# Kernel optimization log

Hardware: AMD Instinct MI355X
Metric: run time of the kernel (lower is better)

The kernel has to match this reference:

```python
import jax, jax.numpy as jnp
import numpy as np

N_NODES = 100000
N_EDGES = 1600000
F_IN, F_HID, F_OUT = 64, 64, 32


def setup_inputs() -> dict:
    key = jax.random.key(0)
    k1, k2, k3, k4 = jax.random.split(key, 4)
    x = jax.random.normal(k1, (N_NODES, F_IN), dtype=jnp.float32)
    edge_idx = jax.random.randint(k2, (2, N_EDGES), 0, N_NODES, dtype=jnp.int64)
    W1 = jax.random.normal(k3, (F_IN, F_HID), dtype=jnp.float32) * (1.0 / np.sqrt(F_IN))
    b1 = jnp.zeros((F_HID,), dtype=jnp.float32)
    W2 = jax.random.normal(k4, (F_HID, F_OUT), dtype=jnp.float32) * (1.0 / np.sqrt(F_HID))
    b2 = jnp.zeros((F_OUT,), dtype=jnp.float32)
    return {"x": x, "edge_idx": edge_idx, "W1": W1, "b1": b1, "W2": W2, "b2": b2}


def _gcn_conv(h, src, dst, norm, W, b, n):
    # PyG GCNConv: transform first, then normalized sum aggregation, then bias.
    h = h @ W                                   # [N, F_out]
    msg = h[src] * norm[:, None]                # [E+N, F_out] gather + scale
    agg = jax.ops.segment_sum(msg, dst, num_segments=n)  # scatter-add
    return agg + b


def reference(x, edge_idx, W1, b1, W2, b2):
    n = x.shape[0]
    loop = jnp.arange(n, dtype=edge_idx.dtype)
    src = jnp.concatenate([edge_idx[0], loop])  # add self-loops
    dst = jnp.concatenate([edge_idx[1], loop])
    # symmetric normalization D^-1/2 (A+I) D^-1/2
    deg = jax.ops.segment_sum(jnp.ones_like(dst, dtype=x.dtype), dst, num_segments=n)
    dinv = jnp.where(deg > 0, jax.lax.rsqrt(deg), 0.0)
    norm = dinv[src] * dinv[dst]                # [E+N]

    h = _gcn_conv(x, src, dst, norm, W1, b1, n)
    h = jax.nn.relu(h)
    # dropout(p=0.5) is identity in eval mode (deterministic reference)
    out = _gcn_conv(h, src, dst, norm, W2, b2, n)
    return out
```

## Files before the change

### kernel.cpp

```cpp
#include <hip/hip_runtime.h>
#include <hip/hip_bf16.h>
#include <hip/hip_fp16.h>


#define N_FEAT_IN 64
#define B2SHIFT 9
#define CHUNK 4096
#define PADSTRIDE 3592

struct alignas(8) half4 { __half2 lo, hi; };
struct alignas(16) half8 { __half2 h[4]; };

__global__ __launch_bounds__(1024) void passA_hist(const int* __restrict__ dst,
                                                   int* __restrict__ H, int E) {
    __shared__ int h[256];
    int t = threadIdx.x;
    if (t < 256) h[t] = 0;
    __syncthreads();
    int base = blockIdx.x * CHUNK;
    int end = min(base + CHUNK, E);
    for (int i = base + t; i < end; i += 1024)
        atomicAdd(&h[dst[i] >> B2SHIFT], 1);
    __syncthreads();
    if (t < 256) H[blockIdx.x * 256 + t] = h[t];
}

__global__ __launch_bounds__(512) void col_scan_a(int* __restrict__ H,
                                                  int* __restrict__ ctot, int NR) {
    __shared__ int s[512];
    int b = blockIdx.x;
    int t = threadIdx.x;
    int v = (t < NR) ? H[t * 256 + b] : 0;
    s[t] = v;
    __syncthreads();
    for (int off = 1; off < 512; off <<= 1) {
        int a = (t >= off) ? s[t - off] : 0;
        __syncthreads();
        s[t] += a;
        __syncthreads();
    }
    if (t < NR) H[t * 256 + b] = s[t] - v;
    if (t == 511) ctot[b] = s[511];
}

__global__ __launch_bounds__(256) void col_scan_b(const int* __restrict__ ctot,
                                                  int* __restrict__ cbase,
                                                  int* __restrict__ bbase,
                                                  int* __restrict__ row_ptr,
                                                  int NB, int n, int E) {
    __shared__ int s[256];
    int t = threadIdx.x;
    int v = ctot[t];
    s[t] = v;
    __syncthreads();
    for (int off = 1; off < 256; off <<= 1) {
        int a = (t >= off) ? s[t - off] : 0;
        __syncthreads();
        s[t] += a;
        __syncthreads();
    }
    int e = s[t] - v;
    cbase[t] = e;
    if (t < NB) bbase[t] = e;
    if (t == 0) { bbase[NB] = E; row_ptr[n] = E; }
}

__global__ __launch_bounds__(1024) void passB_place(const int* __restrict__ src,
                                                    const int* __restrict__ dst,
                                                    const int* __restrict__ H,
                                                    const int* __restrict__ cbase,
                                                    unsigned* __restrict__ bedges, int E) {
    __shared__ int cur[256];
    int t = threadIdx.x;
    if (t < 256) cur[t] = H[blockIdx.x * 256 + t] + cbase[t];
    __syncthreads();
    int base = blockIdx.x * CHUNK;
    int end = min(base + CHUNK, E);
    for (int i = base + t; i < end; i += 1024) {
        int d = dst[i];
        int p = atomicAdd(&cur[d >> B2SHIFT], 1);
        bedges[p] = ((unsigned)src[i] << B2SHIFT) | (unsigned)(d & 511);
    }
}

__global__ __launch_bounds__(1024) void bucket_csr(const int* __restrict__ bbase,
                                                   const unsigned* __restrict__ bedges,
                                                   int* __restrict__ row_ptr,
                                                   int* __restrict__ rend,
                                                   float* __restrict__ dinv,
                                                   int* __restrict__ csr_src, int n) {
    __shared__ int lh[512];
    __shared__ int cur[512];
    int t = threadIdx.x;
    if (t < 512) lh[t] = 0;
    __syncthreads();
    int b = blockIdx.x;
    int beg = bbase[b], end = bbase[b + 1];
    for (int i = beg + t; i < end; i += 1024)
        atomicAdd(&lh[bedges[i] & 511], 1);
    __syncthreads();
    int c = (t < 512) ? lh[t] : 0;
    __syncthreads();
    int cp = (c + 7) & ~7;
    if (t < 512) lh[t] = cp;
    __syncthreads();
    for (int off = 1; off < 512; off <<= 1) {
        int a = (t < 512 && t >= off) ? lh[t - off] : 0;
        __syncthreads();
        if (t < 512) lh[t] += a;
        __syncthreads();
    }
    int pb = ((beg + 7) & ~7) + b * PADSTRIDE;
    if (t < 512) {
        int d = (b << B2SHIFT) + t;
        int rbeg = pb + lh[t] - cp;
        cur[t] = rbeg;
        if (d < n) {
            row_ptr[d] = rbeg;
            rend[d] = rbeg + cp;
            dinv[d] = rsqrtf((float)c + 1.0f);
            for (int i = c; i < cp; ++i) csr_src[rbeg + i] = n;
        }
    }
    __syncthreads();
    for (int i = beg + t; i < end; i += 1024) {
        unsigned v = bedges[i];
        int p = atomicAdd(&cur[v & 511], 1);
        csr_src[p] = (int)(v >> B2SHIFT);
    }
}

__global__ __launch_bounds__(256) void gemm64(const float* __restrict__ A,
                                              const float* __restrict__ W,
                                              const float* __restrict__ dinv,
                                              __half* __restrict__ outh, int n) {
    constexpr int K = 64, FO = 64, CPT = 16;
    __shared__ float As[64][K + 4];
    __shared__ float Ws[K][FO];

    const int t = threadIdx.x;
    const int r0 = blockIdx.x * 64;

    if (blockIdx.x == 0 && t < FO)
        outh[(size_t)n * FO + t] = __float2half(0.f);

    for (int i = t; i < K * FO / 4; i += 256) {
        int k = i / (FO / 4);
        int c4 = (i % (FO / 4)) * 4;
        *(float4*)&Ws[k][c4] = *(const float4*)&W[k * FO + c4];
    }
    for (int i = t; i < 1024; i += 256) {
        int row = i / 16;
        int c4 = (i % 16) * 4;
        int g = r0 + row;
        float4 v = make_float4(0.f, 0.f, 0.f, 0.f);
        if (g < n) v = *(const float4*)&A[(size_t)g * K + c4];
        *(float4*)&As[row][c4] = v;
    }
    __syncthreads();

    const int row = t >> 2;
    const int c0 = (t & 3) * CPT;
    float acc[CPT];
#pragma unroll
    for (int j = 0; j < CPT; ++j) acc[j] = 0.f;
#pragma unroll
    for (int k = 0; k < K; ++k) {
        float xv = As[row][k];
#pragma unroll
        for (int j = 0; j < CPT; ++j) acc[j] = fmaf(xv, Ws[k][c0 + j], acc[j]);
    }

    int g = r0 + row;
    if (g < n) {
        float sc = dinv[g];
#pragma unroll
        for (int j4 = 0; j4 < CPT; j4 += 4) {
            half4 h;
            h.lo = __floats2half2_rn(acc[j4] * sc, acc[j4 + 1] * sc);
            h.hi = __floats2half2_rn(acc[j4 + 2] * sc, acc[j4 + 3] * sc);
            *(half4*)&outh[(size_t)g * FO + c0 + j4] = h;
        }
    }
}

#define ACC8(v)                                                       \
    {                                                                 \
        float2 f0 = __half22float2((v).h[0]);                         \
        float2 f1 = __half22float2((v).h[1]);                         \
        float2 f2 = __half22float2((v).h[2]);                         \
        float2 f3 = __half22float2((v).h[3]);                         \
        a0 += f0.x; a1 += f0.y; a2 += f1.x; a3 += f1.y;               \
        a4 += f2.x; a5 += f2.y; a6 += f3.x; a7 += f3.y;               \
    }

__global__ __launch_bounds__(256) void agg64(const int* __restrict__ row_ptr,
                                             const int* __restrict__ rend,
                                             const int* __restrict__ csr_src,
                                             const float* __restrict__ dinv,
                                             const __half* __restrict__ xs1,
                                             const float* __restrict__ b1,
                                             __half* __restrict__ th, int n) {
    int d = blockIdx.x * 32 + (threadIdx.x >> 3);
    if (d >= n) return;
    int c = threadIdx.x & 7;
    const half8* __restrict__ xrow = (const half8*)xs1 + c;

    half8 sv = xrow[(size_t)d * 8];
    float a0, a1, a2, a3, a4, a5, a6, a7;
    {
        float2 f0 = __half22float2(sv.h[0]), f1 = __half22float2(sv.h[1]);
        float2 f2 = __half22float2(sv.h[2]), f3 = __half22float2(sv.h[3]);
        a0 = f0.x; a1 = f0.y; a2 = f1.x; a3 = f1.y;
        a4 = f2.x; a5 = f2.y; a6 = f3.x; a7 = f3.y;
    }

    int beg = row_ptr[d];
    int end = rend[d];
    if (beg < end) {
        int4 ia = *(const int4*)&csr_src[beg];
        int4 ib = *(const int4*)&csr_src[beg + 4];
        int jb = beg;
        for (;;) {
            int jn = jb + 8;
            bool more = jn < end;
            int js = more ? jn : beg;
            int4 na = *(const int4*)&csr_src[js];
            int4 nb = *(const int4*)&csr_src[js + 4];
            half8 v0 = xrow[(size_t)ia.x * 8];
            half8 v1 = xrow[(size_t)ia.y * 8];
            half8 v2 = xrow[(size_t)ia.z * 8];
            half8 v3 = xrow[(size_t)ia.w * 8];
            half8 v4 = xrow[(size_t)ib.x * 8];
            half8 v5 = xrow[(size_t)ib.y * 8];
            half8 v6 = xrow[(size_t)ib.z * 8];
            half8 v7 = xrow[(size_t)ib.w * 8];
            ACC8(v0); ACC8(v1); ACC8(v2); ACC8(v3);
            ACC8(v4); ACC8(v5); ACC8(v6); ACC8(v7);
            if (!more) break;
            jb = jn; ia = na; ib = nb;
        }
    }

    float di = dinv[d];
    float4 ba = *(const float4*)&b1[8 * c];
    float4 bb = *(const float4*)&b1[8 * c + 4];
    float t0 = fmaxf(fmaf(di, a0, ba.x), 0.f);
    float t1 = fmaxf(fmaf(di, a1, ba.y), 0.f);
    float t2 = fmaxf(fmaf(di, a2, ba.z), 0.f);
    float t3 = fmaxf(fmaf(di, a3, ba.w), 0.f);
    float t4 = fmaxf(fmaf(di, a4, bb.x), 0.f);
    float t5 = fmaxf(fmaf(di, a5, bb.y), 0.f);
    float t6 = fmaxf(fmaf(di, a6, bb.z), 0.f);
    float t7 = fmaxf(fmaf(di, a7, bb.w), 0.f);
    half8 o;
    o.h[0] = __floats2half2_rn(t0, t1);
    o.h[1] = __floats2half2_rn(t2, t3);
    o.h[2] = __floats2half2_rn(t4, t5);
    o.h[3] = __floats2half2_rn(t6, t7);
    *(half8*)&th[(size_t)d * 64 + 8 * c] = o;
}

__global__ __launch_bounds__(256) void gemm32h(const __half* __restrict__ Ah,
                                               const float* __restrict__ W,
                                               const float* __restrict__ dinv,
                                               __half* __restrict__ outh, int n) {
    constexpr int K = 64, FO = 32, CPT = 8;
    __shared__ float As[64][K + 4];
    __shared__ float Ws[K][FO];

    const int t = threadIdx.x;
    const int r0 = blockIdx.x * 64;

    if (blockIdx.x == 0 && t < FO)
        outh[(size_t)n * FO + t] = __float2half(0.f);

    for (int i = t; i < K * FO / 4; i += 256) {
        int k = i / (FO / 4);
        int c4 = (i % (FO / 4)) * 4;
        *(float4*)&Ws[k][c4] = *(const float4*)&W[k * FO + c4];
    }
    for (int i = t; i < 1024; i += 256) {
        int row = i / 16;
        int c4 = (i % 16) * 4;
        int g = r0 + row;
        float4 v = make_float4(0.f, 0.f, 0.f, 0.f);
        if (g < n) {
            half4 hv = *(const half4*)&Ah[(size_t)g * K + c4];
            float2 lo = __half22float2(hv.lo), hi = __half22float2(hv.hi);
            v = make_float4(lo.x, lo.y, hi.x, hi.y);
        }
        *(float4*)&As[row][c4] = v;
    }
    __syncthreads();

    const int row = t >> 2;
    const int c0 = (t & 3) * CPT;
    float acc[CPT];
#pragma unroll
    for (int j = 0; j < CPT; ++j) acc[j] = 0.f;
#pragma unroll
    for (int k = 0; k < K; ++k) {
        float xv = As[row][k];
#pragma unroll
        for (int j = 0; j < CPT; ++j) acc[j] = fmaf(xv, Ws[k][c0 + j], acc[j]);
    }

    int g = r0 + row;
    if (g < n) {
        float sc = dinv[g];
#pragma unroll
        for (int j4 = 0; j4 < CPT; j4 += 4) {
            half4 h;
            h.lo = __floats2half2_rn(acc[j4] * sc, acc[j4 + 1] * sc);
            h.hi = __floats2half2_rn(acc[j4 + 2] * sc, acc[j4 + 3] * sc);
            *(half4*)&outh[(size_t)g * FO + c0 + j4] = h;
        }
    }
}

__global__ __launch_bounds__(256) void agg32(const int* __restrict__ row_ptr,
                                             const int* __restrict__ rend,
                                             const int* __restrict__ csr_src,
                                             const float* __restrict__ dinv,
                                             const __half* __restrict__ xs2,
                                             const float* __restrict__ b2,
                                             float* __restrict__ out, int n) {
    int d = blockIdx.x * 64 + (threadIdx.x >> 2);
    if (d >= n) return;
    int c = threadIdx.x & 3;
    const half8* __restrict__ xrow = (const half8*)xs2 + c;

    half8 sv = xrow[(size_t)d * 4];
    float a0, a1, a2, a3, a4, a5, a6, a7;
    {
        float2 f0 = __half22float2(sv.h[0]), f1 = __half22float2(sv.h[1]);
        float2 f2 = __half22float2(sv.h[2]), f3 = __half22float2(sv.h[3]);
        a0 = f0.x; a1 = f0.y; a2 = f1.x; a3 = f1.y;
        a4 = f2.x; a5 = f2.y; a6 = f3.x; a7 = f3.y;
    }

    int beg = row_ptr[d];
    int end = rend[d];
    if (beg < end) {
        int4 ia = *(const int4*)&csr_src[beg];
        int4 ib = *(const int4*)&csr_src[beg + 4];
        int jb = beg;
        for (;;) {
            int jn = jb + 8;
            bool more = jn < end;
            int js = more ? jn : beg;
            int4 na = *(const int4*)&csr_src[js];
            int4 nb = *(const int4*)&csr_src[js + 4];
            half8 v0 = xrow[(size_t)ia.x * 4];
            half8 v1 = xrow[(size_t)ia.y * 4];
            half8 v2 = xrow[(size_t)ia.z * 4];
            half8 v3 = xrow[(size_t)ia.w * 4];
            half8 v4 = xrow[(size_t)ib.x * 4];
            half8 v5 = xrow[(size_t)ib.y * 4];
            half8 v6 = xrow[(size_t)ib.z * 4];
            half8 v7 = xrow[(size_t)ib.w * 4];
            ACC8(v0); ACC8(v1); ACC8(v2); ACC8(v3);
            ACC8(v4); ACC8(v5); ACC8(v6); ACC8(v7);
            if (!more) break;
            jb = jn; ia = na; ib = nb;
        }
    }

    float di = dinv[d];
    float4 ba = *(const float4*)&b2[8 * c];
    float4 bb = *(const float4*)&b2[8 * c + 4];
    float4 r0, r1;
    r0.x = fmaf(di, a0, ba.x);
    r0.y = fmaf(di, a1, ba.y);
    r0.z = fmaf(di, a2, ba.z);
    r0.w = fmaf(di, a3, ba.w);
    r1.x = fmaf(di, a4, bb.x);
    r1.y = fmaf(di, a5, bb.y);
    r1.z = fmaf(di, a6, bb.z);
    r1.w = fmaf(di, a7, bb.w);
    *(float4*)&out[(size_t)d * 32 + 8 * c] = r0;
    *(float4*)&out[(size_t)d * 32 + 8 * c + 4] = r1;
}

extern "C" void kernel_launch(void* const* d_in, const int* in_sizes, int n_in,
                              void* d_out, int out_size, void* d_ws, size_t ws_size,
                              hipStream_t stream) {
    const float* x  = (const float*)d_in[0];
    const int*   ei = (const int*)d_in[1];
    const float* W1 = (const float*)d_in[2];
    const float* b1 = (const float*)d_in[3];
    const float* W2 = (const float*)d_in[4];
    const float* b2 = (const float*)d_in[5];
    float* out = (float*)d_out;

    const int n = in_sizes[0] / N_FEAT_IN;
    const int E = in_sizes[1] / 2;
    const int* srcI = ei;
    const int* dstI = ei + E;

    const int NB = (n + 511) >> B2SHIFT;
    const int NR = (E + CHUNK - 1) / CHUNK;

    char* ws = (char*)d_ws;
    size_t off = 0;
    auto alloc = [&](size_t bytes) {
        void* p = ws + off;
        off += (bytes + 255) & ~(size_t)255;
        return p;
    };
    float*    dinv    = (float*)alloc((size_t)n * 4);
    int*      row_ptr = (int*)alloc((size_t)(n + 1) * 4);
    int*      rend    = (int*)alloc((size_t)n * 4);
    int*      bbase   = (int*)alloc((size_t)(NB + 1) * 4);
    int*      ctot    = (int*)alloc((size_t)256 * 4);
    int*      cbase   = (int*)alloc((size_t)256 * 4);
    int*      H       = (int*)alloc((size_t)NR * 256 * 4);
    unsigned* bedges  = (unsigned*)alloc((size_t)E * 4);
    int*      csr_src = (int*)alloc((size_t)(E + (size_t)NB * PADSTRIDE + 16) * 4);
    __half*   xs1     = (__half*)alloc((size_t)(n + 1) * 64 * 2);
    __half*   th      = (__half*)alloc((size_t)n * 64 * 2);
    __half*   xs2     = (__half*)alloc((size_t)(n + 1) * 32 * 2);

    passA_hist<<<NR, 1024, 0, stream>>>(dstI, H, E);
    col_scan_a<<<256, 512, 0, stream>>>(H, ctot, NR);
    col_scan_b<<<1, 256, 0, stream>>>(ctot, cbase, bbase, row_ptr, NB, n, E);
    passB_place<<<NR, 1024, 0, stream>>>(srcI, dstI, H, cbase, bedges, E);

    bucket_csr<<<NB, 1024, 0, stream>>>(bbase, bedges, row_ptr, rend, dinv, csr_src, n);

    gemm64<<<(n + 63) / 64, 256, 0, stream>>>(x, W1, dinv, xs1, n);

    agg64<<<(n + 31) / 32, 256, 0, stream>>>(row_ptr, rend, csr_src, dinv, xs1, b1, th, n);

    gemm32h<<<(n + 63) / 64, 256, 0, stream>>>(th, W2, dinv, xs2, n);

    agg32<<<(n + 63) / 64, 256, 0, stream>>>(row_ptr, rend, csr_src, dinv, xs2, b2, out, n);
}
```

Baseline: 204.9 us.

## Replace scan-based bucket placement with atomic fixed-capacity buckets and register-tiled GEMMs

```diff
diff --git a/kernel.cpp b/kernel.cpp
--- a/kernel.cpp
+++ b/kernel.cpp
@@ -6,14 +6,22 @@
 #define N_FEAT_IN 64
 #define B2SHIFT 9
 #define CHUNK 4096
-#define PADSTRIDE 3592
+#define CAP 12288
+#define CSRCAP 16384
 
 struct alignas(8) half4 { __half2 lo, hi; };
 struct alignas(16) half8 { __half2 h[4]; };
 
-__global__ __launch_bounds__(1024) void passA_hist(const int* __restrict__ dst,
-                                                   int* __restrict__ H, int E) {
+__global__ __launch_bounds__(256) void init_k(int* __restrict__ gcur) {
+    gcur[threadIdx.x] = 0;
+}
+
+__global__ __launch_bounds__(1024) void place_k(const int* __restrict__ src,
+                                                const int* __restrict__ dst,
+                                                int* __restrict__ gcur,
+                                                unsigned* __restrict__ bedges, int E) {
     __shared__ int h[256];
+    __shared__ int cur[256];
     int t = threadIdx.x;
     if (t < 256) h[t] = 0;
     __syncthreads();
@@ -22,60 +30,12 @@
     for (int i = base + t; i < end; i += 1024)
         atomicAdd(&h[dst[i] >> B2SHIFT], 1);
     __syncthreads();
-    if (t < 256) H[blockIdx.x * 256 + t] = h[t];
-}
-
-__global__ __launch_bounds__(512) void col_scan_a(int* __restrict__ H,
-                                                  int* __restrict__ ctot, int NR) {
-    __shared__ int s[512];
-    int b = blockIdx.x;
-    int t = threadIdx.x;
-    int v = (t < NR) ? H[t * 256 + b] : 0;
-    s[t] = v;
-    __syncthreads();
-    for (int off = 1; off < 512; off <<= 1) {
-        int a = (t >= off) ? s[t - off] : 0;
-        __syncthreads();
-        s[t] += a;
-        __syncthreads();
-    }
-    if (t < NR) H[t * 256 + b] = s[t] - v;
-    if (t == 511) ctot[b] = s[511];
-}
-
-__global__ __launch_bounds__(256) void col_scan_b(const int* __restrict__ ctot,
-                                                  int* __restrict__ cbase,
-                                                  int* __restrict__ bbase,
-                                                  int* __restrict__ row_ptr,
-                                                  int NB, int n, int E) {
-    __shared__ int s[256];
-    int t = threadIdx.x;
-    int v = ctot[t];
-    s[t] = v;
-    __syncthreads();
-    for (int off = 1; off < 256; off <<= 1) {
-        int a = (t >= off) ? s[t - off] : 0;
-        __syncthreads();
-        s[t] += a;
-        __syncthreads();
-    }
-    int e = s[t] - v;
-    cbase[t] = e;
-    if (t < NB) bbase[t] = e;
-    if (t == 0) { bbase[NB] = E; row_ptr[n] = E; }
-}
-
-__global__ __launch_bounds__(1024) void passB_place(const int* __restrict__ src,
-                                                    const int* __restrict__ dst,
-                                                    const int* __restrict__ H,
-                                                    const int* __restrict__ cbase,
-                                                    unsigned* __restrict__ bedges, int E) {
-    __shared__ int cur[256];
-    int t = threadIdx.x;
-    if (t < 256) cur[t] = H[blockIdx.x * 256 + t] + cbase[t];
-    __syncthreads();
-    int base = blockIdx.x * CHUNK;
-    int end = min(base + CHUNK, E);
+    if (t < 256) {
+        int cnt = h[t];
+        int b0 = cnt ? atomicAdd(&gcur[t], cnt) : 0;
+        cur[t] = t * CAP + b0;
+    }
+    __syncthreads();
     for (int i = base + t; i < end; i += 1024) {
         int d = dst[i];
         int p = atomicAdd(&cur[d >> B2SHIFT], 1);
@@ -83,7 +43,7 @@
     }
 }
 
-__global__ __launch_bounds__(1024) void bucket_csr(const int* __restrict__ bbase,
+__global__ __launch_bounds__(1024) void bucket_csr(const int* __restrict__ gcnt,
                                                    const unsigned* __restrict__ bedges,
                                                    int* __restrict__ row_ptr,
                                                    int* __restrict__ rend,
@@ -95,7 +55,8 @@
     if (t < 512) lh[t] = 0;
     __syncthreads();
     int b = blockIdx.x;
-    int beg = bbase[b], end = bbase[b + 1];
+    int beg = b * CAP;
+    int end = beg + gcnt[b];
     for (int i = beg + t; i < end; i += 1024)
         atomicAdd(&lh[bedges[i] & 511], 1);
     __syncthreads();
@@ -110,7 +71,7 @@
         if (t < 512) lh[t] += a;
         __syncthreads();
     }
-    int pb = ((beg + 7) & ~7) + b * PADSTRIDE;
+    int pb = b * CSRCAP;
     if (t < 512) {
         int d = (b << B2SHIFT) + t;
         int rbeg = pb + lh[t] - cp;
@@ -134,52 +95,66 @@
                                               const float* __restrict__ W,
                                               const float* __restrict__ dinv,
                                               __half* __restrict__ outh, int n) {
-    constexpr int K = 64, FO = 64, CPT = 16;
-    __shared__ float As[64][K + 4];
-    __shared__ float Ws[K][FO];
+    __shared__ float AsT[64][132];
+    __shared__ float Ws[64][64];
 
     const int t = threadIdx.x;
-    const int r0 = blockIdx.x * 64;
-
-    if (blockIdx.x == 0 && t < FO)
-        outh[(size_t)n * FO + t] = __float2half(0.f);
-
-    for (int i = t; i < K * FO / 4; i += 256) {
-        int k = i / (FO / 4);
-        int c4 = (i % (FO / 4)) * 4;
-        *(float4*)&Ws[k][c4] = *(const float4*)&W[k * FO + c4];
-    }
-    for (int i = t; i < 1024; i += 256) {
-        int row = i / 16;
-        int c4 = (i % 16) * 4;
+    const int r0 = blockIdx.x * 128;
+
+    if (blockIdx.x == 0 && t < 64)
+        outh[(size_t)n * 64 + t] = __float2half(0.f);
+
+    for (int i = t; i < 64 * 16; i += 256) {
+        int k = i >> 4;
+        int c4 = (i & 15) * 4;
+        *(float4*)&Ws[k][c4] = *(const float4*)&W[k * 64 + c4];
+    }
+    for (int i = t; i < 128 * 16; i += 256) {
+        int row = i >> 4;
+        int c4 = (i & 15) * 4;
         int g = r0 + row;
         float4 v = make_float4(0.f, 0.f, 0.f, 0.f);
-        if (g < n) v = *(const float4*)&A[(size_t)g * K + c4];
-        *(float4*)&As[row][c4] = v;
-    }
-    __syncthreads();
-
-    const int row = t >> 2;
-    const int c0 = (t & 3) * CPT;
-    float acc[CPT];
-#pragma unroll
-    for (int j = 0; j < CPT; ++j) acc[j] = 0.f;
-#pragma unroll
-    for (int k = 0; k < K; ++k) {
-        float xv = As[row][k];
-#pragma unroll
-        for (int j = 0; j < CPT; ++j) acc[j] = fmaf(xv, Ws[k][c0 + j], acc[j]);
-    }
-
-    int g = r0 + row;
-    if (g < n) {
-        float sc = dinv[g];
-#pragma unroll
-        for (int j4 = 0; j4 < CPT; j4 += 4) {
-            half4 h;
-            h.lo = __floats2half2_rn(acc[j4] * sc, acc[j4 + 1] * sc);
-            h.hi = __floats2half2_rn(acc[j4 + 2] * sc, acc[j4 + 3] * sc);
-            *(half4*)&outh[(size_t)g * FO + c0 + j4] = h;
+        if (g < n) v = *(const float4*)&A[(size_t)g * 64 + c4];
+        AsT[c4 + 0][row] = v.x;
+        AsT[c4 + 1][row] = v.y;
+        AsT[c4 + 2][row] = v.z;
+        AsT[c4 + 3][row] = v.w;
+    }
+    __syncthreads();
+
+    const int rg = t >> 3;
+    const int cg = t & 7;
+    float acc[4][8];
+#pragma unroll
+    for (int r = 0; r < 4; ++r)
+#pragma unroll
+        for (int j = 0; j < 8; ++j) acc[r][j] = 0.f;
+
+#pragma unroll 4
+    for (int k = 0; k < 64; ++k) {
+        float4 a = *(const float4*)&AsT[k][rg * 4];
+        float4 w0 = *(const float4*)&Ws[k][cg * 8];
+        float4 w1 = *(const float4*)&Ws[k][cg * 8 + 4];
+        float av[4] = {a.x, a.y, a.z, a.w};
+        float wv[8] = {w0.x, w0.y, w0.z, w0.w, w1.x, w1.y, w1.z, w1.w};
+#pragma unroll
+        for (int r = 0; r < 4; ++r)
+#pragma unroll
+            for (int j = 0; j < 8; ++j)
+                acc[r][j] = fmaf(av[r], wv[j], acc[r][j]);
+    }
+
+#pragma unroll
+    for (int r = 0; r < 4; ++r) {
+        int g = r0 + rg * 4 + r;
+        if (g < n) {
+            float sc = dinv[g];
+            half8 h;
+            h.h[0] = __floats2half2_rn(acc[r][0] * sc, acc[r][1] * sc);
+            h.h[1] = __floats2half2_rn(acc[r][2] * sc, acc[r][3] * sc);
+            h.h[2] = __floats2half2_rn(acc[r][4] * sc, acc[r][5] * sc);
+            h.h[3] = __floats2half2_rn(acc[r][6] * sc, acc[r][7] * sc);
+            *(half8*)&outh[(size_t)g * 64 + cg * 8] = h;
         }
     }
 }
@@ -265,56 +240,72 @@
                                                const float* __restrict__ W,
                                                const float* __restrict__ dinv,
                                                __half* __restrict__ outh, int n) {
-    constexpr int K = 64, FO = 32, CPT = 8;
-    __shared__ float As[64][K + 4];
-    __shared__ float Ws[K][FO];
+    __shared__ float AsT[64][260];
+    __shared__ float Ws[64][32];
 
     const int t = threadIdx.x;
-    const int r0 = blockIdx.x * 64;
-
-    if (blockIdx.x == 0 && t < FO)
-        outh[(size_t)n * FO + t] = __float2half(0.f);
-
-    for (int i = t; i < K * FO / 4; i += 256) {
-        int k = i / (FO / 4);
-        int c4 = (i % (FO / 4)) * 4;
-        *(float4*)&Ws[k][c4] = *(const float4*)&W[k * FO + c4];
-    }
-    for (int i = t; i < 1024; i += 256) {
-        int row = i / 16;
-        int c4 = (i % 16) * 4;
+    const int r0 = blockIdx.x * 256;
+
+    if (blockIdx.x == 0 && t < 32)
+        outh[(size_t)n * 32 + t] = __float2half(0.f);
+
+    for (int i = t; i < 64 * 8; i += 256) {
+        int k = i >> 3;
+        int c4 = (i & 7) * 4;
+        *(float4*)&Ws[k][c4] = *(const float4*)&W[k * 32 + c4];
+    }
+    for (int i = t; i < 256 * 8; i += 256) {
+        int row = i >> 3;
+        int c8 = (i & 7) * 8;
         int g = r0 + row;
-        float4 v = make_float4(0.f, 0.f, 0.f, 0.f);
         if (g < n) {
-            half4 hv = *(const half4*)&Ah[(size_t)g * K + c4];
-            float2 lo = __half22float2(hv.lo), hi = __half22float2(hv.hi);
-            v = make_float4(lo.x, lo.y, hi.x, hi.y);
-        }
-        *(float4*)&As[row][c4] = v;
-    }
-    __syncthreads();
-
-    const int row = t >> 2;
-    const int c0 = (t & 3) * CPT;
-    float acc[CPT];
-#pragma unroll
-    for (int j = 0; j < CPT; ++j) acc[j] = 0.f;
-#pragma unroll
-    for (int k = 0; k < K; ++k) {
-        float xv = As[row][k];
-#pragma unroll
-        for (int j = 0; j < CPT; ++j) acc[j] = fmaf(xv, Ws[k][c0 + j], acc[j]);
-    }
-
-    int g = r0 + row;
-    if (g < n) {
-        float sc = dinv[g];
-#pragma unroll
-        for (int j4 = 0; j4 < CPT; j4 += 4) {
-            half4 h;
-            h.lo = __floats2half2_rn(acc[j4] * sc, acc[j4 + 1] * sc);
-            h.hi = __floats2half2_rn(acc[j4 + 2] * sc, acc[j4 + 3] * sc);
-            *(half4*)&outh[(size_t)g * FO + c0 + j4] = h;
+            half8 hv = *(const half8*)&Ah[(size_t)g * 64 + c8];
+            float2 f0 = __half22float2(hv.h[0]), f1 = __half22float2(hv.h[1]);
+            float2 f2 = __half22float2(hv.h[2]), f3 = __half22float2(hv.h[3]);
+            AsT[c8 + 0][row] = f0.x; AsT[c8 + 1][row] = f0.y;
+            AsT[c8 + 2][row] = f1.x; AsT[c8 + 3][row] = f1.y;
+            AsT[c8 + 4][row] = f2.x; AsT[c8 + 5][row] = f2.y;
+            AsT[c8 + 6][row] = f3.x; AsT[c8 + 7][row] = f3.y;
+        } else {
+#pragma unroll
+            for (int j = 0; j < 8; ++j) AsT[c8 + j][row] = 0.f;
+        }
+    }
+    __syncthreads();
+
+    const int rg = t >> 2;
+    const int cg = t & 3;
+    float acc[4][8];
+#pragma unroll
+    for (int r = 0; r < 4; ++r)
+#pragma unroll
+        for (int j = 0; j < 8; ++j) acc[r][j] = 0.f;
+
+#pragma unroll 4
+    for (int k = 0; k < 64; ++k) {
+        float4 a = *(const float4*)&AsT[k][rg * 4];
+        float4 w0 = *(const float4*)&Ws[k][cg * 8];
+        float4 w1 = *(const float4*)&Ws[k][cg * 8 + 4];
+        float av[4] = {a.x, a.y, a.z, a.w};
+        float wv[8] = {w0.x, w0.y, w0.z, w0.w, w1.x, w1.y, w1.z, w1.w};
+#pragma unroll
+        for (int r = 0; r < 4; ++r)
+#pragma unroll
+            for (int j = 0; j < 8; ++j)
+                acc[r][j] = fmaf(av[r], wv[j], acc[r][j]);
+    }
+
+#pragma unroll
+    for (int r = 0; r < 4; ++r) {
+        int g = r0 + rg * 4 + r;
+        if (g < n) {
+            float sc = dinv[g];
+            half8 h;
+            h.h[0] = __floats2half2_rn(acc[r][0] * sc, acc[r][1] * sc);
+            h.h[1] = __floats2half2_rn(acc[r][2] * sc, acc[r][3] * sc);
+            h.h[2] = __floats2half2_rn(acc[r][4] * sc, acc[r][5] * sc);
+            h.h[3] = __floats2half2_rn(acc[r][6] * sc, acc[r][7] * sc);
+            *(half8*)&outh[(size_t)g * 32 + cg * 8] = h;
         }
     }
 }
@@ -412,28 +403,22 @@
     float*    dinv    = (float*)alloc((size_t)n * 4);
     int*      row_ptr = (int*)alloc((size_t)(n + 1) * 4);
     int*      rend    = (int*)alloc((size_t)n * 4);
-    int*      bbase   = (int*)alloc((size_t)(NB + 1) * 4);
-    int*      ctot    = (int*)alloc((size_t)256 * 4);
-    int*      cbase   = (int*)alloc((size_t)256 * 4);
-    int*      H       = (int*)alloc((size_t)NR * 256 * 4);
-    unsigned* bedges  = (unsigned*)alloc((size_t)E * 4);
-    int*      csr_src = (int*)alloc((size_t)(E + (size_t)NB * PADSTRIDE + 16) * 4);
+    int*      gcur    = (int*)alloc((size_t)256 * 4);
+    unsigned* bedges  = (unsigned*)alloc((size_t)NB * CAP * 4);
+    int*      csr_src = (int*)alloc((size_t)NB * CSRCAP * 4);
     __half*   xs1     = (__half*)alloc((size_t)(n + 1) * 64 * 2);
     __half*   th      = (__half*)alloc((size_t)n * 64 * 2);
     __half*   xs2     = (__half*)alloc((size_t)(n + 1) * 32 * 2);
 
-    passA_hist<<<NR, 1024, 0, stream>>>(dstI, H, E);
-    col_scan_a<<<256, 512, 0, stream>>>(H, ctot, NR);
-    col_scan_b<<<1, 256, 0, stream>>>(ctot, cbase, bbase, row_ptr, NB, n, E);
-    passB_place<<<NR, 1024, 0, stream>>>(srcI, dstI, H, cbase, bedges, E);
-
-    bucket_csr<<<NB, 1024, 0, stream>>>(bbase, bedges, row_ptr, rend, dinv, csr_src, n);
-
-    gemm64<<<(n + 63) / 64, 256, 0, stream>>>(x, W1, dinv, xs1, n);
+    init_k<<<1, 256, 0, stream>>>(gcur);
+    place_k<<<NR, 1024, 0, stream>>>(srcI, dstI, gcur, bedges, E);
+    bucket_csr<<<NB, 1024, 0, stream>>>(gcur, bedges, row_ptr, rend, dinv, csr_src, n);
+
+    gemm64<<<(n + 127) / 128, 256, 0, stream>>>(x, W1, dinv, xs1, n);
 
     agg64<<<(n + 31) / 32, 256, 0, stream>>>(row_ptr, rend, csr_src, dinv, xs1, b1, th, n);
 
-    gemm32h<<<(n + 63) / 64, 256, 0, stream>>>(th, W2, dinv, xs2, n);
+    gemm32h<<<(n + 255) / 256, 256, 0, stream>>>(th, W2, dinv, xs2, n);
 
     agg32<<<(n + 63) / 64, 256, 0, stream>>>(row_ptr, rend, csr_src, dinv, xs2, b2, out, n);
 }
```

Result: faster. 198.5 us (median of 2 runs) (-3.1%).
